# Kernel tuning notes

Hardware: AMD Instinct MI355X
Metric: run time of the kernel (lower is better)

Reference implementation:

```python
import jax, jax.numpy as jnp
import numpy as np

B, H, W, C = 2, 64, 64, 192
DM = int(2.0 * C)   # d_inner = ssm_ratio * hidden_dim = 384
N = 16              # d_state
R = 12              # dt_rank = ceil(C / 16)
K = 4               # scan directions


def _ln(x, g, b, eps):
    mu = jnp.mean(x, axis=-1, keepdims=True)
    var = jnp.var(x, axis=-1, keepdims=True)
    return (x - mu) * jax.lax.rsqrt(var + eps) * g + b


def setup_inputs() -> dict:
    key = jax.random.key(0)
    ks = jax.random.split(key, 8)
    return {
        "input": jax.random.normal(ks[0], (B, H, W, C), jnp.float32),
        "norm_g": jnp.ones((C,), jnp.float32),
        "norm_b": jnp.zeros((C,), jnp.float32),
        "in_proj_w": jax.random.normal(ks[1], (C, 2 * DM), jnp.float32) * 0.02,
        "conv_w": jax.random.normal(ks[2], (DM, 1, 3, 3), jnp.float32) * 0.1,
        "conv_b": jnp.zeros((DM,), jnp.float32),
        "x_proj_w": jax.random.normal(ks[3], (K, R + 2 * N, DM), jnp.float32) * 0.02,
        "dt_w": jax.random.normal(ks[4], (K, DM, R), jnp.float32) * 0.1,
        "dt_b": jax.random.uniform(ks[5], (K, DM), jnp.float32, -4.0, -2.0),
        "A_logs": jnp.tile(jnp.log(jnp.arange(1, N + 1, dtype=jnp.float32))[None, None, :], (K, DM, 1)),
        "Ds": jnp.ones((K, DM), jnp.float32),
        "out_norm_g": jnp.ones((DM,), jnp.float32),
        "out_norm_b": jnp.zeros((DM,), jnp.float32),
        "out_proj_w": jax.random.normal(ks[6], (DM, C), jnp.float32) * 0.02,
    }


def _selective_scan(us, deltas, A, Bs, Cs):
    # us, deltas: (B,K,D,L); A: (K,D,N); Bs, Cs: (B,K,N,L)
    u_l = jnp.moveaxis(us, -1, 0)       # (L,B,K,D)
    d_l = jnp.moveaxis(deltas, -1, 0)   # (L,B,K,D)
    B_l = jnp.moveaxis(Bs, -1, 0)       # (L,B,K,N)
    C_l = jnp.moveaxis(Cs, -1, 0)       # (L,B,K,N)
    h0 = jnp.zeros(us.shape[:3] + (A.shape[-1],), us.dtype)  # (B,K,D,N)

    def step(h, xs):
        u_t, d_t, b_t, c_t = xs
        dA = jnp.exp(d_t[..., None] * A)                       # (B,K,D,N)
        h = dA * h + (d_t * u_t)[..., None] * b_t[:, :, None, :]
        y = jnp.einsum('bkdn,bkn->bkd', h, c_t)
        return h, y

    _, ys = jax.lax.scan(step, h0, (u_l, d_l, B_l, C_l))
    return jnp.moveaxis(ys, 0, -1)  # (B,K,D,L)


def reference(input, norm_g, norm_b, in_proj_w, conv_w, conv_b, x_proj_w,
              dt_w, dt_b, A_logs, Ds, out_norm_g, out_norm_b, out_proj_w):
    Bz, Hh, Ww, Cc = input.shape
    L = Hh * Ww
    # pre-norm
    xn = _ln(input, norm_g, norm_b, 1e-6)
    # input projection -> x, z
    xz = xn @ in_proj_w                      # (B,H,W,2*DM)
    x, z = jnp.split(xz, 2, axis=-1)
    # depthwise conv + SiLU (channels-first)
    x = jnp.transpose(x, (0, 3, 1, 2))       # (B,DM,H,W)
    Dm = x.shape[1]
    x = jax.lax.conv_general_dilated(
        x, conv_w, (1, 1), 'SAME',
        dimension_numbers=('NCHW', 'OIHW', 'NCHW'),
        feature_group_count=Dm) + conv_b[None, :, None, None]
    x = jax.nn.silu(x)
    # 4-direction cross-scan: hw, wh, and their reverses
    x_flat = x.reshape(Bz, Dm, L)
    x_t = jnp.transpose(x, (0, 1, 3, 2)).reshape(Bz, Dm, L)
    xs = jnp.stack([x_flat, x_t], axis=1)                  # (B,2,DM,L)
    xs = jnp.concatenate([xs, jnp.flip(xs, -1)], axis=1)   # (B,4,DM,L)
    Rr = dt_w.shape[2]
    Nn = A_logs.shape[2]
    x_dbl = jnp.einsum('bkdl,kcd->bkcl', xs, x_proj_w)     # (B,4,R+2N,L)
    dts, Bs, Cs = jnp.split(x_dbl, [Rr, Rr + Nn], axis=2)
    deltas = jax.nn.softplus(
        jnp.einsum('bkrl,kdr->bkdl', dts, dt_w) + dt_b[None, :, :, None])
    A = -jnp.exp(A_logs)                                   # (4,DM,N)
    out_y = _selective_scan(xs, deltas, A, Bs, Cs) + Ds[None, :, :, None] * xs
    # merge the 4 directions back
    inv = jnp.flip(out_y[:, 2:], -1)

    def wh(t):
        return jnp.transpose(t.reshape(Bz, Dm, Ww, Hh), (0, 1, 3, 2)).reshape(Bz, Dm, L)

    y = out_y[:, 0] + inv[:, 0] + wh(out_y[:, 1]) + wh(inv[:, 1])  # (B,DM,L)
    y = jnp.transpose(y, (0, 2, 1))                                # (B,L,DM)
    y = _ln(y, out_norm_g, out_norm_b, 1e-5).reshape(Bz, Hh, Ww, Dm)
    y = y * jax.nn.silu(z)
    out = y @ out_proj_w
    # residual (drop_path=0 -> identity)
    return input + out
```

## Files before the change

kernel.cpp:

```cpp
#include <hip/hip_runtime.h>
#include <hip/hip_bf16.h>
#include <hip/hip_fp16.h>


typedef __attribute__((ext_vector_type(8))) short short8;
typedef __attribute__((ext_vector_type(4))) float floatx4;

__global__ __launch_bounds__(256) void k_ln(const float* __restrict__ in,
                                            const float* __restrict__ g,
                                            const float* __restrict__ be,
                                            __hip_bfloat16* __restrict__ out) {
  int row = blockIdx.x * 4 + (threadIdx.x >> 6);
  int lane = threadIdx.x & 63;
  const float* x = in + (long)row * 192;
  float v0 = x[lane], v1 = x[lane + 64], v2 = x[lane + 128];
  float s = v0 + v1 + v2;
  float s2 = v0 * v0 + v1 * v1 + v2 * v2;
  #pragma unroll
  for (int o = 32; o > 0; o >>= 1) { s += __shfl_xor(s, o); s2 += __shfl_xor(s2, o); }
  float mu = s * (1.f / 192.f);
  float var = s2 * (1.f / 192.f) - mu * mu;
  float r = rsqrtf(var + 1e-6f);
  __hip_bfloat16* op = out + (long)row * 192;
  op[lane]       = __float2bfloat16((v0 - mu) * r * g[lane]       + be[lane]);
  op[lane + 64]  = __float2bfloat16((v1 - mu) * r * g[lane + 64]  + be[lane + 64]);
  op[lane + 128] = __float2bfloat16((v2 - mu) * r * g[lane + 128] + be[lane + 128]);
}

__global__ __launch_bounds__(256) void k_packw(const float* __restrict__ ipw,
                                               const float* __restrict__ xpw,
                                               const float* __restrict__ opw,
                                               __hip_bfloat16* __restrict__ Wt1,
                                               __hip_bfloat16* __restrict__ Wt2,
                                               __hip_bfloat16* __restrict__ Wt3) {
  int idx = blockIdx.x * 256 + threadIdx.x;
  if (idx < 147456) {
    int n = idx / 192, k = idx - n * 192;
    Wt1[idx] = __float2bfloat16(ipw[(long)k * 768 + n]);
  } else if (idx < 147456 + 73728) {
    int t = idx - 147456;
    int j = t / 384;
    float v = (j < 176) ? xpw[t] : 0.f;
    Wt2[t] = __float2bfloat16(v);
  } else if (idx < 147456 + 73728 + 73728) {
    int t = idx - 147456 - 73728;
    int n = t / 384, k = t - n * 384;
    Wt3[t] = __float2bfloat16(opw[(long)k * 192 + n]);
  }
}

__device__ __forceinline__ int inv_dir(int k, int p) {
  int pt = ((p & 63) << 6) | (p >> 6);
  if (k == 0) return p;
  if (k == 1) return pt;
  if (k == 2) return 4095 - p;
  return 4095 - pt;
}
__device__ __forceinline__ int dir_pix(int k, int l) { return inv_dir(k, l); }

template <int EPI, int TN>
__global__ __launch_bounds__(256) void k_gemm_mfma(const __hip_bfloat16* __restrict__ A,
                                                   const __hip_bfloat16* __restrict__ Bt,
                                                   const float* __restrict__ Res,
                                                   float* __restrict__ Co,
                                                   __hip_bfloat16* __restrict__ CoB,
                                                   __hip_bfloat16* __restrict__ Co2B,
                                                   float* __restrict__ dtsS,
                                                   float* __restrict__ BCs,
                                                   int M, int N, int Kk) {
  constexpr int NI = TN / 32;
  __shared__ __align__(16) short As[64 * 64];
  __shared__ __align__(16) short Bs[TN * 64];
  int tid = threadIdx.x;
  int wave = tid >> 6, lane = tid & 63;
  int mlane = lane & 15, quad = lane >> 4;
  int row0 = blockIdx.y * 64, col0 = blockIdx.x * TN;
  int wr = wave & 1, wc = wave >> 1;
  floatx4 acc[2][NI];
  #pragma unroll
  for (int mi = 0; mi < 2; mi++)
    #pragma unroll
    for (int ni = 0; ni < NI; ni++) acc[mi][ni] = (floatx4){0.f, 0.f, 0.f, 0.f};

  for (int k0 = 0; k0 < Kk; k0 += 64) {
    #pragma unroll
    for (int c = tid; c < 512; c += 256) {
      int r = c >> 3, j = c & 7;
      *(float4*)&As[r * 64 + ((j ^ (r & 7)) << 3)] =
          *(const float4*)&A[(long)(row0 + r) * Kk + k0 + j * 8];
    }
    #pragma unroll
    for (int c = tid; c < TN * 8; c += 256) {
      int r = c >> 3, j = c & 7;
      *(float4*)&Bs[r * 64 + ((j ^ (r & 7)) << 3)] =
          *(const float4*)&Bt[(long)(col0 + r) * Kk + k0 + j * 8];
    }
    __syncthreads();
    short8 af[2][2], bf[NI][2];
    #pragma unroll
    for (int mi = 0; mi < 2; mi++) {
      int r = wr * 32 + mi * 16 + mlane;
      #pragma unroll
      for (int kk = 0; kk < 2; kk++) {
        int jx = (kk * 4 + quad) ^ (r & 7);
        af[mi][kk] = *(const short8*)&As[r * 64 + jx * 8];
      }
    }
    #pragma unroll
    for (int ni = 0; ni < NI; ni++) {
      int rn = wc * (TN / 2) + ni * 16 + mlane;
      #pragma unroll
      for (int kk = 0; kk < 2; kk++) {
        int jx = (kk * 4 + quad) ^ (rn & 7);
        bf[ni][kk] = *(const short8*)&Bs[rn * 64 + jx * 8];
      }
    }
    #pragma unroll
    for (int kk = 0; kk < 2; kk++)
      #pragma unroll
      for (int mi = 0; mi < 2; mi++)
        #pragma unroll
        for (int ni = 0; ni < NI; ni++)
          acc[mi][ni] = __builtin_amdgcn_mfma_f32_16x16x32_bf16(af[mi][kk], bf[ni][kk],
                                                                acc[mi][ni], 0, 0, 0);
    __syncthreads();
  }
  #pragma unroll
  for (int mi = 0; mi < 2; mi++) {
    #pragma unroll
    for (int ni = 0; ni < NI; ni++) {
      int cc = col0 + wc * (TN / 2) + ni * 16 + mlane;
      #pragma unroll
      for (int i = 0; i < 4; i++) {
        int rr = row0 + wr * 32 + mi * 16 + quad * 4 + i;
        float v = acc[mi][ni][i];
        if (EPI == 1) {
          Co[(long)rr * N + cc] = v + Res[(long)rr * N + cc];
        } else if (EPI == 2) {
          if (cc < 384) CoB[(long)rr * 384 + cc] = __float2bfloat16(v);
          else          Co2B[(long)rr * 384 + (cc - 384)] = __float2bfloat16(v);
        } else {
          if (cc < 176) {
            int k4 = (cc >= 132) ? 3 : (cc >= 88) ? 2 : (cc >= 44) ? 1 : 0;
            int c = cc - k4 * 44;
            int b = rr >> 12, p = rr & 4095;
            long lbase = ((long)((b << 2) + k4) << 12) + p;
            if (c < 12) dtsS[lbase * 12 + c] = v;
            else        BCs[lbase * 32 + (c - 12)] = v;
          }
        }
      }
    }
  }
}

__global__ __launch_bounds__(384) void k_conv(const __hip_bfloat16* __restrict__ xbufB,
                                              const float* __restrict__ cw,
                                              const float* __restrict__ cb,
                                              __hip_bfloat16* __restrict__ xcb) {
  int blk = blockIdx.x;
  int wg = blk & 15, h = (blk >> 4) & 63, b = blk >> 10;
  int w0 = wg * 4;
  int d = threadIdx.x;
  float wt[9];
  const float* wp = cw + d * 9;
  #pragma unroll
  for (int i = 0; i < 9; i++) wt[i] = wp[i];
  float bias = cb[d];
  float v[3][6];
  #pragma unroll
  for (int r = 0; r < 3; r++) {
    int hh = h + r - 1;
    bool rok = (hh >= 0) && (hh < 64);
    #pragma unroll
    for (int c = 0; c < 6; c++) {
      int ww = w0 + c - 1;
      bool ok = rok && (ww >= 0) && (ww < 64);
      v[r][c] = ok ? __bfloat162float(xbufB[((long)(b << 12) + (hh << 6) + ww) * 384 + d]) : 0.f;
    }
  }
  #pragma unroll
  for (int i = 0; i < 4; i++) {
    float acc = bias;
    #pragma unroll
    for (int r = 0; r < 3; r++)
      #pragma unroll
      for (int c = 0; c < 3; c++)
        acc += v[r][i + c] * wt[r * 3 + c];
    float sg = 1.f / (1.f + __expf(-acc));
    xcb[((long)(b << 12) + (h << 6) + (w0 + i)) * 384 + d] = __float2bfloat16(acc * sg);
  }
}

__global__ __launch_bounds__(384) void k_dt(const float* __restrict__ dtsS,
                                            const float* __restrict__ dt_w,
                                            const float* __restrict__ dt_b,
                                            __half* __restrict__ dpre) {
  int bid = blockIdx.x;
  int chunk = bid & 127, bk = bid >> 7;
  int k = bk & 3;
  int d = threadIdx.x;
  float w[12];
  const float* dwp = dt_w + ((long)(k * 384) + d) * 12;
  #pragma unroll
  for (int r = 0; r < 12; r++) w[r] = dwp[r];
  float db = dt_b[k * 384 + d];
  long base = ((long)bk << 12) + chunk * 32;
  #pragma unroll 4
  for (int t = 0; t < 32; t++) {
    const float4* dq = (const float4*)(dtsS + (base + t) * 12);
    float4 q0 = dq[0], q1 = dq[1], q2 = dq[2];
    float x = db + q0.x * w[0] + q0.y * w[1] + q0.z * w[2] + q0.w * w[3]
                 + q1.x * w[4] + q1.y * w[5] + q1.z * w[6] + q1.w * w[7]
                 + q2.x * w[8] + q2.y * w[9] + q2.z * w[10] + q2.w * w[11];
    float e = __expf(x);
    float delta = (x > 15.f) ? x : __logf(1.f + e);
    dpre[(base + t) * 384 + d] = __float2half(delta);
  }
}

__device__ __forceinline__ void pow16(float r, float* pws) {
  pws[0] = r;
  #pragma unroll
  for (int n = 1; n < 16; n++) {
    int m = n + 1, c = (m + 1) / 2, f = m - c;
    pws[n] = pws[c - 1] * pws[f - 1];
  }
}

__global__ __launch_bounds__(384) void k_scan0(
    const __half* __restrict__ dpre, const float* __restrict__ BCs,
    const __hip_bfloat16* __restrict__ xcb,
    const float* __restrict__ A_logs,
    float* __restrict__ Eb, float* __restrict__ Dend) {
  int bid = blockIdx.x;
  int s = bid & 127, bk = bid >> 7;
  int k = bk & 3, b = bk >> 2;
  int d = threadIdx.x;
  const float* al = A_logs + ((long)(k * 384) + d) * 16;
  bool pw = true;
  float av[16];
  #pragma unroll
  for (int n = 0; n < 16; n++) {
    float a = __expf(al[n]);
    av[n] = -a;
    pw = pw && (fabsf(a - (float)(n + 1)) < 1e-3f);
  }
  float h[16];
  #pragma unroll
  for (int n = 0; n < 16; n++) h[n] = 0.f;
  float cum = 0.f;
  long bpk = (long)bk << 12;
  long bpix = (long)(b << 12);

  if (pw) {
    #pragma unroll 4
    for (int t = 0; t < 32; t++) {
      int p = dir_pix(k, s * 32 + t);
      float delta = __half2float(dpre[(bpk + p) * 384 + d]);
      float u = __bfloat162float(xcb[(bpix + p) * 384 + d]);
      cum += delta;
      float du = delta * u;
      float rr = __expf(-delta);
      float pws[16]; pow16(rr, pws);
      const float4* Bq = (const float4*)(BCs + (bpk + p) * 32);
      float4 b0 = Bq[0], b1 = Bq[1], b2 = Bq[2], b3 = Bq[3];
      float Bl[16] = {b0.x, b0.y, b0.z, b0.w, b1.x, b1.y, b1.z, b1.w,
                      b2.x, b2.y, b2.z, b2.w, b3.x, b3.y, b3.z, b3.w};
      #pragma unroll
      for (int n = 0; n < 16; n++) h[n] = pws[n] * h[n] + du * Bl[n];
    }
  } else {
    for (int t = 0; t < 32; t++) {
      int p = dir_pix(k, s * 32 + t);
      float delta = __half2float(dpre[(bpk + p) * 384 + d]);
      float u = __bfloat162float(xcb[(bpix + p) * 384 + d]);
      cum += delta;
      float du = delta * u;
      const float4* Bq = (const float4*)(BCs + (bpk + p) * 32);
      float4 b0 = Bq[0], b1 = Bq[1], b2 = Bq[2], b3 = Bq[3];
      float Bl[16] = {b0.x, b0.y, b0.z, b0.w, b1.x, b1.y, b1.z, b1.w,
                      b2.x, b2.y, b2.z, b2.w, b3.x, b3.y, b3.z, b3.w};
      #pragma unroll
      for (int n = 0; n < 16; n++) {
        float dA = __expf(delta * av[n]);
        h[n] = dA * h[n] + du * Bl[n];
      }
    }
  }
  long g = (long)bk * 128 + s;
  float* Ep = Eb + g * 6144 + d * 16;
  #pragma unroll
  for (int n = 0; n < 16; n++) Ep[n] = h[n];
  Dend[g * 384 + d] = cum;
}

__global__ __launch_bounds__(128) void k_combine(float* __restrict__ Eb,
                                                 const float* __restrict__ Dend,
                                                 const float* __restrict__ A_logs) {
  int bid = blockIdx.x;
  int bk = bid / 384;
  int d = bid - bk * 384;
  int k = bk & 3;
  int s = threadIdx.x;
  const float* al = A_logs + ((long)(k * 384) + d) * 16;
  bool pw = true;
  float av[16];
  #pragma unroll
  for (int n = 0; n < 16; n++) {
    float a = __expf(al[n]);
    av[n] = -a;
    pw = pw && (fabsf(a - (float)(n + 1)) < 1e-3f);
  }

  long ebase = ((long)bk * 128 + s) * 6144 + d * 16;
  float e[16];
  *(float4*)&e[0]  = *(const float4*)&Eb[ebase + 0];
  *(float4*)&e[4]  = *(const float4*)&Eb[ebase + 4];
  *(float4*)&e[8]  = *(const float4*)&Eb[ebase + 8];
  *(float4*)&e[12] = *(const float4*)&Eb[ebase + 12];
  float sig = Dend[((long)bk * 128 + s) * 384 + d];

  __shared__ float sE[128][17];
  sE[s][0] = sig;
  #pragma unroll
  for (int n = 0; n < 16; n++) sE[s][1 + n] = e[n];
  __syncthreads();

  for (int o = 1; o < 128; o <<= 1) {
    float ps = 0.f, pe[16];
    bool act = (s >= o);
    if (act) {
      ps = sE[s - o][0];
      #pragma unroll
      for (int n = 0; n < 16; n++) pe[n] = sE[s - o][1 + n];
    }
    __syncthreads();
    if (act) {
      if (pw) {
        float rc = __expf(-sig);
        float pwr[16]; pow16(rc, pwr);
        #pragma unroll
        for (int n = 0; n < 16; n++) e[n] += pwr[n] * pe[n];
      } else {
        #pragma unroll
        for (int n = 0; n < 16; n++) e[n] += __expf(av[n] * sig) * pe[n];
      }
      sig += ps;
      sE[s][0] = sig;
      #pragma unroll
      for (int n = 0; n < 16; n++) sE[s][1 + n] = e[n];
    }
    __syncthreads();
  }

  float ho[16];
  if (s == 0) {
    #pragma unroll
    for (int n = 0; n < 16; n++) ho[n] = 0.f;
  } else {
    #pragma unroll
    for (int n = 0; n < 16; n++) ho[n] = sE[s - 1][1 + n];
  }
  *(float4*)&Eb[ebase + 0]  = *(float4*)&ho[0];
  *(float4*)&Eb[ebase + 4]  = *(float4*)&ho[4];
  *(float4*)&Eb[ebase + 8]  = *(float4*)&ho[8];
  *(float4*)&Eb[ebase + 12] = *(float4*)&ho[12];
}

template <int ATOMIC>
__global__ __launch_bounds__(384) void k_scan1(
    const __half* __restrict__ dpre, const float* __restrict__ BCs,
    const __hip_bfloat16* __restrict__ xcb,
    const float* __restrict__ A_logs, const float* __restrict__ Eb,
    __hip_bfloat16* __restrict__ ybufB, float* __restrict__ ysum) {
  int bid = blockIdx.x;
  int s = bid & 127, bk = bid >> 7;
  int k = bk & 3, b = bk >> 2;
  int d = threadIdx.x;
  const float* al = A_logs + ((long)(k * 384) + d) * 16;
  bool pw = true;
  float av[16];
  #pragma unroll
  for (int n = 0; n < 16; n++) {
    float a = __expf(al[n]);
    av[n] = -a;
    pw = pw && (fabsf(a - (float)(n + 1)) < 1e-3f);
  }
  float h[16];
  const float* hp = Eb + ((long)bk * 128 + s) * 6144 + d * 16;
  #pragma unroll
  for (int n = 0; n < 16; n++) h[n] = hp[n];
  long bpk = (long)bk << 12;
  long bpix = (long)(b << 12);

  if (pw) {
    #pragma unroll 4
    for (int t = 0; t < 32; t++) {
      int p = dir_pix(k, s * 32 + t);
      float delta = __half2float(dpre[(bpk + p) * 384 + d]);
      float u = __bfloat162float(xcb[(bpix + p) * 384 + d]);
      float du = delta * u;
      float rr = __expf(-delta);
      float pws[16]; pow16(rr, pws);
      const float4* Bq = (const float4*)(BCs + (bpk + p) * 32);
      float4 b0 = Bq[0], b1 = Bq[1], b2 = Bq[2], b3 = Bq[3];
      float Bl[16] = {b0.x, b0.y, b0.z, b0.w, b1.x, b1.y, b1.z, b1.w,
                      b2.x, b2.y, b2.z, b2.w, b3.x, b3.y, b3.z, b3.w};
      const float4* Cq = Bq + 4;
      float4 c0 = Cq[0], c1 = Cq[1], c2 = Cq[2], c3 = Cq[3];
      float Cl[16] = {c0.x, c0.y, c0.z, c0.w, c1.x, c1.y, c1.z, c1.w,
                      c2.x, c2.y, c2.z, c2.w, c3.x, c3.y, c3.z, c3.w};
      float y = 0.f;
      #pragma unroll
      for (int n = 0; n < 16; n++) { h[n] = pws[n] * h[n] + du * Bl[n]; y += h[n] * Cl[n]; }
      if (ATOMIC) atomicAdd(&ysum[(bpix + p) * 384 + d], y);
      else        ybufB[(bpk + p) * 384 + d] = __float2bfloat16(y);
    }
  } else {
    for (int t = 0; t < 32; t++) {
      int p = dir_pix(k, s * 32 + t);
      float delta = __half2float(dpre[(bpk + p) * 384 + d]);
      float u = __bfloat162float(xcb[(bpix + p) * 384 + d]);
      float du = delta * u;
      const float4* Bq = (const float4*)(BCs + (bpk + p) * 32);
      float4 b0 = Bq[0], b1 = Bq[1], b2 = Bq[2], b3 = Bq[3];
      float Bl[16] = {b0.x, b0.y, b0.z, b0.w, b1.x, b1.y, b1.z, b1.w,
                      b2.x, b2.y, b2.z, b2.w, b3.x, b3.y, b3.z, b3.w};
      const float4* Cq = Bq + 4;
      float4 c0 = Cq[0], c1 = Cq[1], c2 = Cq[2], c3 = Cq[3];
      float Cl[16] = {c0.x, c0.y, c0.z, c0.w, c1.x, c1.y, c1.z, c1.w,
                      c2.x, c2.y, c2.z, c2.w, c3.x, c3.y, c3.z, c3.w};
      float y = 0.f;
      #pragma unroll
      for (int n = 0; n < 16; n++) {
        float dA = __expf(delta * av[n]);
        h[n] = dA * h[n] + du * Bl[n];
        y += h[n] * Cl[n];
      }
      if (ATOMIC) atomicAdd(&ysum[(bpix + p) * 384 + d], y);
      else        ybufB[(bpk + p) * 384 + d] = __float2bfloat16(y);
    }
  }
}

template <int GATHER>
__global__ __launch_bounds__(384) void k_merge(const __hip_bfloat16* __restrict__ yinB,
                                               const float* __restrict__ yinF,
                                               const __hip_bfloat16* __restrict__ xcb,
                                               const __hip_bfloat16* __restrict__ zbufB,
                                               const float* __restrict__ Ds,
                                               const float* __restrict__ g,
                                               const float* __restrict__ be,
                                               __hip_bfloat16* __restrict__ yactb) {
  int row = blockIdx.x;
  int d = threadIdx.x;
  float v;
  if (GATHER) {
    int b = row >> 12, p = row & 4095;
    long base = ((long)(b << 2) << 12) + p;
    v = __bfloat162float(yinB[base * 384 + d])
      + __bfloat162float(yinB[(base + 4096) * 384 + d])
      + __bfloat162float(yinB[(base + 8192) * 384 + d])
      + __bfloat162float(yinB[(base + 12288) * 384 + d]);
  } else {
    v = yinF[(long)row * 384 + d];
  }
  float sd = Ds[d] + Ds[384 + d] + Ds[768 + d] + Ds[1152 + d];
  v += __bfloat162float(xcb[(long)row * 384 + d]) * sd;
  float s1 = v, s2 = v * v;
  #pragma unroll
  for (int o = 32; o > 0; o >>= 1) { s1 += __shfl_xor(s1, o); s2 += __shfl_xor(s2, o); }
  __shared__ float r1[6], r2[6];
  int wv = threadIdx.x >> 6;
  if ((threadIdx.x & 63) == 0) { r1[wv] = s1; r2[wv] = s2; }
  __syncthreads();
  float S1 = 0.f, S2 = 0.f;
  #pragma unroll
  for (int i = 0; i < 6; i++) { S1 += r1[i]; S2 += r2[i]; }
  float mu = S1 * (1.f / 384.f);
  float var = S2 * (1.f / 384.f) - mu * mu;
  float rr = rsqrtf(var + 1e-5f);
  float yn = (v - mu) * rr * g[d] + be[d];
  float z = __bfloat162float(zbufB[(long)row * 384 + d]);
  float sg = z / (1.f + __expf(-z));
  yactb[(long)row * 384 + d] = __float2bfloat16(yn * sg);
}

extern "C" void kernel_launch(void* const* d_in, const int* in_sizes, int n_in,
                              void* d_out, int out_size, void* d_ws, size_t ws_size,
                              hipStream_t stream) {
  const float* input      = (const float*)d_in[0];
  const float* norm_g     = (const float*)d_in[1];
  const float* norm_b     = (const float*)d_in[2];
  const float* in_proj_w  = (const float*)d_in[3];
  const float* conv_w     = (const float*)d_in[4];
  const float* conv_b     = (const float*)d_in[5];
  const float* x_proj_w   = (const float*)d_in[6];
  const float* dt_w       = (const float*)d_in[7];
  const float* dt_b       = (const float*)d_in[8];
  const float* A_logs     = (const float*)d_in[9];
  const float* Ds         = (const float*)d_in[10];
  const float* out_norm_g = (const float*)d_in[11];
  const float* out_norm_b = (const float*)d_in[12];
  const float* out_proj_w = (const float*)d_in[13];
  float* out = (float*)d_out;

  bool big = ws_size >= (size_t)27934720 * 4;

  float* ws = (float*)d_ws;
  long o = 0;
  __hip_bfloat16* xnb   = (__hip_bfloat16*)(ws + o); o += 786432;
  __hip_bfloat16* xbufB = (__hip_bfloat16*)(ws + o); o += 1572864;
  __hip_bfloat16* zbufB = (__hip_bfloat16*)(ws + o); o += 1572864;
  __hip_bfloat16* xcb   = (__hip_bfloat16*)(ws + o); o += 1572864;
  __hip_bfloat16* Wt1   = (__hip_bfloat16*)(ws + o); o += 73728;
  __hip_bfloat16* Wt2   = (__hip_bfloat16*)(ws + o); o += 36864;
  __hip_bfloat16* Wt3   = (__hip_bfloat16*)(ws + o); o += 36864;
  float* dtsS           = ws + o;                    o += 393216;
  float* BCs            = ws + o;                    o += 1048576;
  __half* dpre          = (__half*)(ws + o);         o += 6291456;
  float* Eb             = ws + o;                    o += 6291456;
  float* Dend           = ws + o;                    o += 393216;
  __hip_bfloat16* ybufB = (__hip_bfloat16*)(ws + o);
  float* ysum           = ws + o;                    o += big ? 6291456 : 3145728;
  __hip_bfloat16* yactb = (__hip_bfloat16*)(ws + o); o += 1572864;

  k_ln<<<dim3(2048), dim3(256), 0, stream>>>(input, norm_g, norm_b, xnb);
  k_packw<<<dim3(1152), dim3(256), 0, stream>>>(in_proj_w, x_proj_w, out_proj_w, Wt1, Wt2, Wt3);
  k_gemm_mfma<2, 128><<<dim3(6, 128), dim3(256), 0, stream>>>(xnb, Wt1, nullptr, nullptr, xbufB, zbufB,
                                                              nullptr, nullptr, 8192, 768, 192);
  k_conv<<<dim3(2048), dim3(384), 0, stream>>>(xbufB, conv_w, conv_b, xcb);
  k_gemm_mfma<3, 64><<<dim3(3, 128), dim3(256), 0, stream>>>(xcb, Wt2, nullptr, nullptr, nullptr, nullptr,
                                                             dtsS, BCs, 8192, 192, 384);
  k_dt<<<dim3(1024), dim3(384), 0, stream>>>(dtsS, dt_w, dt_b, dpre);
  k_scan0<<<dim3(1024), dim3(384), 0, stream>>>(dpre, BCs, xcb, A_logs, Eb, Dend);
  k_combine<<<dim3(3072), dim3(128), 0, stream>>>(Eb, Dend, A_logs);
  if (big) {
    k_scan1<0><<<dim3(1024), dim3(384), 0, stream>>>(dpre, BCs, xcb, A_logs, Eb, ybufB, nullptr);
    k_merge<1><<<dim3(8192), dim3(384), 0, stream>>>(ybufB, nullptr, xcb, zbufB, Ds,
                                                     out_norm_g, out_norm_b, yactb);
  } else {
    hipMemsetAsync(ysum, 0, (size_t)3145728 * 4, stream);
    k_scan1<1><<<dim3(1024), dim3(384), 0, stream>>>(dpre, BCs, xcb, A_logs, Eb, nullptr, ysum);
    k_merge<0><<<dim3(8192), dim3(384), 0, stream>>>(nullptr, ysum, xcb, zbufB, Ds,
                                                     out_norm_g, out_norm_b, yactb);
  }
  k_gemm_mfma<1, 64><<<dim3(3, 128), dim3(256), 0, stream>>>(yactb, Wt3, input, out, nullptr, nullptr,
                                                             nullptr, nullptr, 8192, 192, 384);
}
```

Before: 244.2 us.

## Fuse chunked scan passes into single kernel with decoupled look-back prefix

Replaces the three-kernel chunked selective scan (local pass, block-level combine, second pass) with one kernel. It uses dynamic tile IDs from an atomic counter and a decoupled look-back over status flags to chain chunk states across blocks. Delta, u and B/C values from the first pass are kept in registers and shared memory and reused in the second pass, so they are not re-read from global memory. The small-workspace atomic path is dropped, so ybufB is now always allocated. This adds spin-waiting between blocks and higher register pressure from the packed register caches.

```diff
diff --git a/kernel.cpp b/kernel.cpp
--- a/kernel.cpp
+++ b/kernel.cpp
@@ -228,15 +228,20 @@
   }
 }
 
-__global__ __launch_bounds__(384) void k_scan0(
+__global__ __launch_bounds__(384) void k_scan(
     const __half* __restrict__ dpre, const float* __restrict__ BCs,
-    const __hip_bfloat16* __restrict__ xcb,
-    const float* __restrict__ A_logs,
-    float* __restrict__ Eb, float* __restrict__ Dend) {
-  int bid = blockIdx.x;
-  int s = bid & 127, bk = bid >> 7;
+    const __hip_bfloat16* __restrict__ xcb, const float* __restrict__ A_logs,
+    float* __restrict__ Epart, float* __restrict__ cumPart,
+    float* __restrict__ Hincl, float* __restrict__ sigIncl,
+    int* __restrict__ status, __hip_bfloat16* __restrict__ ybufB) {
+  __shared__ __align__(16) float sBC[32 * 32];
+  __shared__ int smTile;
+  int d = threadIdx.x;
+  if (d == 0) smTile = atomicAdd(status + 1024, 1);
+  __syncthreads();
+  int tile = smTile;
+  int bk = tile & 7, s = tile >> 3;
   int k = bk & 3, b = bk >> 2;
-  int d = threadIdx.x;
   const float* al = A_logs + ((long)(k * 384) + d) * 16;
   bool pw = true;
   float av[16];
@@ -246,207 +251,188 @@
     av[n] = -a;
     pw = pw && (fabsf(a - (float)(n + 1)) < 1e-3f);
   }
+  int l0 = s * 32;
+  int p0 = dir_pix(k, l0);
+  int stride = dir_pix(k, l0 + 1) - p0;
+  long bpk = (long)bk << 12;
+  long bpix = (long)(b << 12);
+  const unsigned short* dpu = (const unsigned short*)dpre;
+  const unsigned short* xcu = (const unsigned short*)xcb;
+
   float h[16];
   #pragma unroll
   for (int n = 0; n < 16; n++) h[n] = 0.f;
   float cum = 0.f;
-  long bpk = (long)bk << 12;
-  long bpix = (long)(b << 12);
+  unsigned dpk[16], upk[16];
 
   if (pw) {
+    #pragma unroll
+    for (int t = 0; t < 32; t++) {
+      int p = p0 + stride * t;
+      unsigned hd = dpu[(bpk + p) * 384 + d];
+      unsigned ub = xcu[(bpix + p) * 384 + d];
+      if (t & 1) { dpk[t >> 1] |= hd << 16; upk[t >> 1] |= ub << 16; }
+      else       { dpk[t >> 1] = hd;        upk[t >> 1] = ub; }
+      float delta = __half2float(__ushort_as_half((unsigned short)hd));
+      float u = __uint_as_float(ub << 16);
+      cum += delta;
+      float du = delta * u;
+      const float4* Bq = (const float4*)(BCs + (bpk + p) * 32);
+      if (d < 8) ((float4*)sBC)[t * 8 + d] = Bq[d];
+      float4 b0 = Bq[0], b1 = Bq[1], b2 = Bq[2], b3 = Bq[3];
+      float Bl[16] = {b0.x, b0.y, b0.z, b0.w, b1.x, b1.y, b1.z, b1.w,
+                      b2.x, b2.y, b2.z, b2.w, b3.x, b3.y, b3.z, b3.w};
+      float rr = __expf(-delta);
+      float pws[16]; pow16(rr, pws);
+      #pragma unroll
+      for (int n = 0; n < 16; n++) h[n] = pws[n] * h[n] + du * Bl[n];
+    }
+  } else {
     #pragma unroll 4
     for (int t = 0; t < 32; t++) {
-      int p = dir_pix(k, s * 32 + t);
+      int p = p0 + stride * t;
       float delta = __half2float(dpre[(bpk + p) * 384 + d]);
-      float u = __bfloat162float(xcb[(bpix + p) * 384 + d]);
+      float u = __uint_as_float((unsigned)xcu[(bpix + p) * 384 + d] << 16);
       cum += delta;
+      float du = delta * u;
+      const float4* Bq = (const float4*)(BCs + (bpk + p) * 32);
+      if (d < 8) ((float4*)sBC)[t * 8 + d] = Bq[d];
+      float4 b0 = Bq[0], b1 = Bq[1], b2 = Bq[2], b3 = Bq[3];
+      float Bl[16] = {b0.x, b0.y, b0.z, b0.w, b1.x, b1.y, b1.z, b1.w,
+                      b2.x, b2.y, b2.z, b2.w, b3.x, b3.y, b3.z, b3.w};
+      #pragma unroll
+      for (int n = 0; n < 16; n++) h[n] = __expf(delta * av[n]) * h[n] + du * Bl[n];
+    }
+  }
+
+  long tb = (long)tile * 6144 + d * 16;
+  if (s > 0) {
+    *(float4*)&Epart[tb + 0]  = *(float4*)&h[0];
+    *(float4*)&Epart[tb + 4]  = *(float4*)&h[4];
+    *(float4*)&Epart[tb + 8]  = *(float4*)&h[8];
+    *(float4*)&Epart[tb + 12] = *(float4*)&h[12];
+    cumPart[(long)tile * 384 + d] = cum;
+    __syncthreads();
+    if (d == 0) __hip_atomic_store(&status[tile], 1, __ATOMIC_RELEASE, __HIP_MEMORY_SCOPE_AGENT);
+  }
+  float hin[16];
+  #pragma unroll
+  for (int n = 0; n < 16; n++) hin[n] = 0.f;
+  float sig_in = 0.f;
+  if (s > 0) {
+    float sigAcc = 0.f;
+    int j = s - 1;
+    while (true) {
+      int jt = j * 8 + bk;
+      int st;
+      do {
+        st = __hip_atomic_load(&status[jt], __ATOMIC_ACQUIRE, __HIP_MEMORY_SCOPE_AGENT);
+        if (st == 0) __builtin_amdgcn_s_sleep(1);
+      } while (st == 0);
+      float fac[16];
+      if (pw) { float rc = __expf(-sigAcc); pow16(rc, fac); }
+      else {
+        #pragma unroll
+        for (int n = 0; n < 16; n++) fac[n] = __expf(av[n] * sigAcc);
+      }
+      long jb = (long)jt * 6144 + d * 16;
+      if (st == 2) {
+        float Hj[16];
+        *(float4*)&Hj[0]  = *(const float4*)&Hincl[jb + 0];
+        *(float4*)&Hj[4]  = *(const float4*)&Hincl[jb + 4];
+        *(float4*)&Hj[8]  = *(const float4*)&Hincl[jb + 8];
+        *(float4*)&Hj[12] = *(const float4*)&Hincl[jb + 12];
+        #pragma unroll
+        for (int n = 0; n < 16; n++) hin[n] += fac[n] * Hj[n];
+        sig_in = sigAcc + sigIncl[(long)jt * 384 + d];
+        break;
+      } else {
+        float Ej[16];
+        *(float4*)&Ej[0]  = *(const float4*)&Epart[jb + 0];
+        *(float4*)&Ej[4]  = *(const float4*)&Epart[jb + 4];
+        *(float4*)&Ej[8]  = *(const float4*)&Epart[jb + 8];
+        *(float4*)&Ej[12] = *(const float4*)&Epart[jb + 12];
+        #pragma unroll
+        for (int n = 0; n < 16; n++) hin[n] += fac[n] * Ej[n];
+        sigAcc += cumPart[(long)jt * 384 + d];
+        j--;
+        if (j < 0) { sig_in = sigAcc; break; }
+      }
+    }
+  }
+  {
+    float fac[16];
+    if (pw) { float rc = __expf(-cum); pow16(rc, fac); }
+    else {
+      #pragma unroll
+      for (int n = 0; n < 16; n++) fac[n] = __expf(av[n] * cum);
+    }
+    float Hi[16];
+    #pragma unroll
+    for (int n = 0; n < 16; n++) Hi[n] = fac[n] * hin[n] + h[n];
+    *(float4*)&Hincl[tb + 0]  = *(float4*)&Hi[0];
+    *(float4*)&Hincl[tb + 4]  = *(float4*)&Hi[4];
+    *(float4*)&Hincl[tb + 8]  = *(float4*)&Hi[8];
+    *(float4*)&Hincl[tb + 12] = *(float4*)&Hi[12];
+    sigIncl[(long)tile * 384 + d] = sig_in + cum;
+    __syncthreads();
+    if (d == 0) __hip_atomic_store(&status[tile], 2, __ATOMIC_RELEASE, __HIP_MEMORY_SCOPE_AGENT);
+  }
+  float h2[16];
+  #pragma unroll
+  for (int n = 0; n < 16; n++) h2[n] = hin[n];
+  if (pw) {
+    #pragma unroll
+    for (int t = 0; t < 32; t++) {
+      int p = p0 + stride * t;
+      unsigned wd = dpk[t >> 1];
+      unsigned wu = upk[t >> 1];
+      unsigned short hd = (t & 1) ? (unsigned short)(wd >> 16) : (unsigned short)(wd & 0xffff);
+      unsigned ub = (t & 1) ? (wu >> 16) : (wu & 0xffff);
+      float delta = __half2float(__ushort_as_half(hd));
+      float u = __uint_as_float(ub << 16);
       float du = delta * u;
       float rr = __expf(-delta);
       float pws[16]; pow16(rr, pws);
-      const float4* Bq = (const float4*)(BCs + (bpk + p) * 32);
-      float4 b0 = Bq[0], b1 = Bq[1], b2 = Bq[2], b3 = Bq[3];
+      const float4* Rq = (const float4*)&sBC[t * 32];
+      float4 b0 = Rq[0], b1 = Rq[1], b2 = Rq[2], b3 = Rq[3];
+      float4 c0 = Rq[4], c1 = Rq[5], c2 = Rq[6], c3 = Rq[7];
       float Bl[16] = {b0.x, b0.y, b0.z, b0.w, b1.x, b1.y, b1.z, b1.w,
                       b2.x, b2.y, b2.z, b2.w, b3.x, b3.y, b3.z, b3.w};
-      #pragma unroll
-      for (int n = 0; n < 16; n++) h[n] = pws[n] * h[n] + du * Bl[n];
-    }
-  } else {
-    for (int t = 0; t < 32; t++) {
-      int p = dir_pix(k, s * 32 + t);
-      float delta = __half2float(dpre[(bpk + p) * 384 + d]);
-      float u = __bfloat162float(xcb[(bpix + p) * 384 + d]);
-      cum += delta;
-      float du = delta * u;
-      const float4* Bq = (const float4*)(BCs + (bpk + p) * 32);
-      float4 b0 = Bq[0], b1 = Bq[1], b2 = Bq[2], b3 = Bq[3];
-      float Bl[16] = {b0.x, b0.y, b0.z, b0.w, b1.x, b1.y, b1.z, b1.w,
-                      b2.x, b2.y, b2.z, b2.w, b3.x, b3.y, b3.z, b3.w};
-      #pragma unroll
-      for (int n = 0; n < 16; n++) {
-        float dA = __expf(delta * av[n]);
-        h[n] = dA * h[n] + du * Bl[n];
-      }
-    }
-  }
-  long g = (long)bk * 128 + s;
-  float* Ep = Eb + g * 6144 + d * 16;
-  #pragma unroll
-  for (int n = 0; n < 16; n++) Ep[n] = h[n];
-  Dend[g * 384 + d] = cum;
-}
-
-__global__ __launch_bounds__(128) void k_combine(float* __restrict__ Eb,
-                                                 const float* __restrict__ Dend,
-                                                 const float* __restrict__ A_logs) {
-  int bid = blockIdx.x;
-  int bk = bid / 384;
-  int d = bid - bk * 384;
-  int k = bk & 3;
-  int s = threadIdx.x;
-  const float* al = A_logs + ((long)(k * 384) + d) * 16;
-  bool pw = true;
-  float av[16];
-  #pragma unroll
-  for (int n = 0; n < 16; n++) {
-    float a = __expf(al[n]);
-    av[n] = -a;
-    pw = pw && (fabsf(a - (float)(n + 1)) < 1e-3f);
-  }
-
-  long ebase = ((long)bk * 128 + s) * 6144 + d * 16;
-  float e[16];
-  *(float4*)&e[0]  = *(const float4*)&Eb[ebase + 0];
-  *(float4*)&e[4]  = *(const float4*)&Eb[ebase + 4];
-  *(float4*)&e[8]  = *(const float4*)&Eb[ebase + 8];
-  *(float4*)&e[12] = *(const float4*)&Eb[ebase + 12];
-  float sig = Dend[((long)bk * 128 + s) * 384 + d];
-
-  __shared__ float sE[128][17];
-  sE[s][0] = sig;
-  #pragma unroll
-  for (int n = 0; n < 16; n++) sE[s][1 + n] = e[n];
-  __syncthreads();
-
-  for (int o = 1; o < 128; o <<= 1) {
-    float ps = 0.f, pe[16];
-    bool act = (s >= o);
-    if (act) {
-      ps = sE[s - o][0];
-      #pragma unroll
-      for (int n = 0; n < 16; n++) pe[n] = sE[s - o][1 + n];
-    }
-    __syncthreads();
-    if (act) {
-      if (pw) {
-        float rc = __expf(-sig);
-        float pwr[16]; pow16(rc, pwr);
-        #pragma unroll
-        for (int n = 0; n < 16; n++) e[n] += pwr[n] * pe[n];
-      } else {
-        #pragma unroll
-        for (int n = 0; n < 16; n++) e[n] += __expf(av[n] * sig) * pe[n];
-      }
-      sig += ps;
-      sE[s][0] = sig;
-      #pragma unroll
-      for (int n = 0; n < 16; n++) sE[s][1 + n] = e[n];
-    }
-    __syncthreads();
-  }
-
-  float ho[16];
-  if (s == 0) {
-    #pragma unroll
-    for (int n = 0; n < 16; n++) ho[n] = 0.f;
-  } else {
-    #pragma unroll
-    for (int n = 0; n < 16; n++) ho[n] = sE[s - 1][1 + n];
-  }
-  *(float4*)&Eb[ebase + 0]  = *(float4*)&ho[0];
-  *(float4*)&Eb[ebase + 4]  = *(float4*)&ho[4];
-  *(float4*)&Eb[ebase + 8]  = *(float4*)&ho[8];
-  *(float4*)&Eb[ebase + 12] = *(float4*)&ho[12];
-}
-
-template <int ATOMIC>
-__global__ __launch_bounds__(384) void k_scan1(
-    const __half* __restrict__ dpre, const float* __restrict__ BCs,
-    const __hip_bfloat16* __restrict__ xcb,
-    const float* __restrict__ A_logs, const float* __restrict__ Eb,
-    __hip_bfloat16* __restrict__ ybufB, float* __restrict__ ysum) {
-  int bid = blockIdx.x;
-  int s = bid & 127, bk = bid >> 7;
-  int k = bk & 3, b = bk >> 2;
-  int d = threadIdx.x;
-  const float* al = A_logs + ((long)(k * 384) + d) * 16;
-  bool pw = true;
-  float av[16];
-  #pragma unroll
-  for (int n = 0; n < 16; n++) {
-    float a = __expf(al[n]);
-    av[n] = -a;
-    pw = pw && (fabsf(a - (float)(n + 1)) < 1e-3f);
-  }
-  float h[16];
-  const float* hp = Eb + ((long)bk * 128 + s) * 6144 + d * 16;
-  #pragma unroll
-  for (int n = 0; n < 16; n++) h[n] = hp[n];
-  long bpk = (long)bk << 12;
-  long bpix = (long)(b << 12);
-
-  if (pw) {
-    #pragma unroll 4
-    for (int t = 0; t < 32; t++) {
-      int p = dir_pix(k, s * 32 + t);
-      float delta = __half2float(dpre[(bpk + p) * 384 + d]);
-      float u = __bfloat162float(xcb[(bpix + p) * 384 + d]);
-      float du = delta * u;
-      float rr = __expf(-delta);
-      float pws[16]; pow16(rr, pws);
-      const float4* Bq = (const float4*)(BCs + (bpk + p) * 32);
-      float4 b0 = Bq[0], b1 = Bq[1], b2 = Bq[2], b3 = Bq[3];
-      float Bl[16] = {b0.x, b0.y, b0.z, b0.w, b1.x, b1.y, b1.z, b1.w,
-                      b2.x, b2.y, b2.z, b2.w, b3.x, b3.y, b3.z, b3.w};
-      const float4* Cq = Bq + 4;
-      float4 c0 = Cq[0], c1 = Cq[1], c2 = Cq[2], c3 = Cq[3];
       float Cl[16] = {c0.x, c0.y, c0.z, c0.w, c1.x, c1.y, c1.z, c1.w,
                       c2.x, c2.y, c2.z, c2.w, c3.x, c3.y, c3.z, c3.w};
       float y = 0.f;
       #pragma unroll
-      for (int n = 0; n < 16; n++) { h[n] = pws[n] * h[n] + du * Bl[n]; y += h[n] * Cl[n]; }
-      if (ATOMIC) atomicAdd(&ysum[(bpix + p) * 384 + d], y);
-      else        ybufB[(bpk + p) * 384 + d] = __float2bfloat16(y);
+      for (int n = 0; n < 16; n++) { h2[n] = pws[n] * h2[n] + du * Bl[n]; y += h2[n] * Cl[n]; }
+      ybufB[(bpk + p) * 384 + d] = __float2bfloat16(y);
     }
   } else {
+    #pragma unroll 4
     for (int t = 0; t < 32; t++) {
-      int p = dir_pix(k, s * 32 + t);
+      int p = p0 + stride * t;
       float delta = __half2float(dpre[(bpk + p) * 384 + d]);
-      float u = __bfloat162float(xcb[(bpix + p) * 384 + d]);
+      float u = __uint_as_float((unsigned)xcu[(bpix + p) * 384 + d] << 16);
       float du = delta * u;
-      const float4* Bq = (const float4*)(BCs + (bpk + p) * 32);
-      float4 b0 = Bq[0], b1 = Bq[1], b2 = Bq[2], b3 = Bq[3];
+      const float4* Rq = (const float4*)&sBC[t * 32];
+      float4 b0 = Rq[0], b1 = Rq[1], b2 = Rq[2], b3 = Rq[3];
+      float4 c0 = Rq[4], c1 = Rq[5], c2 = Rq[6], c3 = Rq[7];
       float Bl[16] = {b0.x, b0.y, b0.z, b0.w, b1.x, b1.y, b1.z, b1.w,
                       b2.x, b2.y, b2.z, b2.w, b3.x, b3.y, b3.z, b3.w};
-      const float4* Cq = Bq + 4;
-      float4 c0 = Cq[0], c1 = Cq[1], c2 = Cq[2], c3 = Cq[3];
       float Cl[16] = {c0.x, c0.y, c0.z, c0.w, c1.x, c1.y, c1.z, c1.w,
                       c2.x, c2.y, c2.z, c2.w, c3.x, c3.y, c3.z, c3.w};
       float y = 0.f;
       #pragma unroll
       for (int n = 0; n < 16; n++) {
         float dA = __expf(delta * av[n]);
-        h[n] = dA * h[n] + du * Bl[n];
-        y += h[n] * Cl[n];
+        h2[n] = dA * h2[n] + du * Bl[n];
+        y += h2[n] * Cl[n];
       }
-      if (ATOMIC) atomicAdd(&ysum[(bpix + p) * 384 + d], y);
-      else        ybufB[(bpk + p) * 384 + d] = __float2bfloat16(y);
-    }
-  }
-}
-
-template <int GATHER>
+      ybufB[(bpk + p) * 384 + d] = __float2bfloat16(y);
+    }
+  }
+}
+
 __global__ __launch_bounds__(384) void k_merge(const __hip_bfloat16* __restrict__ yinB,
-                                               const float* __restrict__ yinF,
                                                const __hip_bfloat16* __restrict__ xcb,
                                                const __hip_bfloat16* __restrict__ zbufB,
                                                const float* __restrict__ Ds,
@@ -455,17 +441,12 @@
                                                __hip_bfloat16* __restrict__ yactb) {
   int row = blockIdx.x;
   int d = threadIdx.x;
-  float v;
-  if (GATHER) {
-    int b = row >> 12, p = row & 4095;
-    long base = ((long)(b << 2) << 12) + p;
-    v = __bfloat162float(yinB[base * 384 + d])
-      + __bfloat162float(yinB[(base + 4096) * 384 + d])
-      + __bfloat162float(yinB[(base + 8192) * 384 + d])
-      + __bfloat162float(yinB[(base + 12288) * 384 + d]);
-  } else {
-    v = yinF[(long)row * 384 + d];
-  }
+  int b = row >> 12, p = row & 4095;
+  long base = ((long)(b << 2) << 12) + p;
+  float v = __bfloat162float(yinB[base * 384 + d])
+          + __bfloat162float(yinB[(base + 4096) * 384 + d])
+          + __bfloat162float(yinB[(base + 8192) * 384 + d])
+          + __bfloat162float(yinB[(base + 12288) * 384 + d]);
   float sd = Ds[d] + Ds[384 + d] + Ds[768 + d] + Ds[1152 + d];
   v += __bfloat162float(xcb[(long)row * 384 + d]) * sd;
   float s1 = v, s2 = v * v;
@@ -506,8 +487,6 @@
   const float* out_proj_w = (const float*)d_in[13];
   float* out = (float*)d_out;
 
-  bool big = ws_size >= (size_t)27934720 * 4;
-
   float* ws = (float*)d_ws;
   long o = 0;
   __hip_bfloat16* xnb   = (__hip_bfloat16*)(ws + o); o += 786432;
@@ -520,12 +499,15 @@
   float* dtsS           = ws + o;                    o += 393216;
   float* BCs            = ws + o;                    o += 1048576;
   __half* dpre          = (__half*)(ws + o);         o += 6291456;
-  float* Eb             = ws + o;                    o += 6291456;
-  float* Dend           = ws + o;                    o += 393216;
-  __hip_bfloat16* ybufB = (__hip_bfloat16*)(ws + o);
-  float* ysum           = ws + o;                    o += big ? 6291456 : 3145728;
+  float* Epart          = ws + o;                    o += 6291456;
+  float* Hincl          = ws + o;                    o += 6291456;
+  float* cumPart        = ws + o;                    o += 393216;
+  float* sigIncl        = ws + o;                    o += 393216;
+  int*   statusA        = (int*)(ws + o);            o += 2048;
+  __hip_bfloat16* ybufB = (__hip_bfloat16*)(ws + o); o += 6291456;
   __hip_bfloat16* yactb = (__hip_bfloat16*)(ws + o); o += 1572864;
 
+  hipMemsetAsync(statusA, 0, 2048 * 4, stream);
   k_ln<<<dim3(2048), dim3(256), 0, stream>>>(input, norm_g, norm_b, xnb);
   k_packw<<<dim3(1152), dim3(256), 0, stream>>>(in_proj_w, x_proj_w, out_proj_w, Wt1, Wt2, Wt3);
   k_gemm_mfma<2, 128><<<dim3(6, 128), dim3(256), 0, stream>>>(xnb, Wt1, nullptr, nullptr, xbufB, zbufB,
@@ -534,18 +516,9 @@
   k_gemm_mfma<3, 64><<<dim3(3, 128), dim3(256), 0, stream>>>(xcb, Wt2, nullptr, nullptr, nullptr, nullptr,
                                                              dtsS, BCs, 8192, 192, 384);
   k_dt<<<dim3(1024), dim3(384), 0, stream>>>(dtsS, dt_w, dt_b, dpre);
-  k_scan0<<<dim3(1024), dim3(384), 0, stream>>>(dpre, BCs, xcb, A_logs, Eb, Dend);
-  k_combine<<<dim3(3072), dim3(128), 0, stream>>>(Eb, Dend, A_logs);
-  if (big) {
-    k_scan1<0><<<dim3(1024), dim3(384), 0, stream>>>(dpre, BCs, xcb, A_logs, Eb, ybufB, nullptr);
-    k_merge<1><<<dim3(8192), dim3(384), 0, stream>>>(ybufB, nullptr, xcb, zbufB, Ds,
-                                                     out_norm_g, out_norm_b, yactb);
-  } else {
-    hipMemsetAsync(ysum, 0, (size_t)3145728 * 4, stream);
-    k_scan1<1><<<dim3(1024), dim3(384), 0, stream>>>(dpre, BCs, xcb, A_logs, Eb, nullptr, ysum);
-    k_merge<0><<<dim3(8192), dim3(384), 0, stream>>>(nullptr, ysum, xcb, zbufB, Ds,
-                                                     out_norm_g, out_norm_b, yactb);
-  }
+  k_scan<<<dim3(1024), dim3(384), 0, stream>>>(dpre, BCs, xcb, A_logs, Epart, cumPart,
+                                               Hincl, sigIncl, statusA, ybufB);
+  k_merge<<<dim3(8192), dim3(384), 0, stream>>>(ybufB, xcb, zbufB, Ds, out_norm_g, out_norm_b, yactb);
   k_gemm_mfma<1, 64><<<dim3(3, 128), dim3(256), 0, stream>>>(yactb, Wt3, input, out, nullptr, nullptr,
                                                              nullptr, nullptr, 8192, 192, 384);
 }
```

New measurement: 656.6 us. +168.9%, slower.
